# Optimization experiments

Hardware: AMD Instinct MI355X
Metric: run time of the kernel (lower is better)

The kernel has to match this reference:

```python
import jax, jax.numpy as jnp
import numpy as np

B, N, D, DHAT, H = 2, 2048, 1024, 512, 16
F = DHAT // H   # qk head dim = 32
G = D // H      # v head dim = 64


def setup_inputs() -> dict:
    key = jax.random.key(0)
    ks = jax.random.split(key, 9)
    def lin_w(k, din, dout):
        return jax.random.normal(k, (din, dout), jnp.float32) / np.sqrt(din).astype(np.float32)
    return {
        "x": jax.random.normal(ks[0], (B, N, D), jnp.float32),
        "wq": lin_w(ks[1], D, DHAT), "bq": jnp.zeros((DHAT,), jnp.float32),
        "wk": lin_w(ks[2], D, DHAT), "bk": jnp.zeros((DHAT,), jnp.float32),
        "wv": lin_w(ks[3], D, D),    "bv": jnp.zeros((D,), jnp.float32),
        "wo": lin_w(ks[4], D, D),    "bo": jnp.zeros((D,), jnp.float32),
    }


def _phi(x):
    # elu feature map: phi(x) = elu(x) + 1 (strictly positive)
    return jax.nn.elu(x) + 1.0


def _linear_attention(Q, K, V):
    # Q,K: (B,H,N,F); V: (B,H,N,G)
    kv = jnp.cumsum(jnp.einsum('bhtf,bhtg->bhtfg', K, V), axis=2)  # (B,H,N,F,G)
    Z = 1.0 / (jnp.einsum('bhtf,bhtf->bht', Q, jnp.cumsum(K, axis=2)) + 1e-6)
    out = jnp.einsum('bhtf,bhtfg->bhtg', Q, kv) * Z[..., None]     # (B,H,N,G)
    return out


def reference(x, wq, bq, wk, bk, wv, bv, wo, bo):
    Bx, Nx, Dx = x.shape
    Q = (x @ wq + bq).reshape(Bx, Nx, H, F).transpose(0, 2, 1, 3)  # (B,H,N,F)
    K = (x @ wk + bk).reshape(Bx, Nx, H, F).transpose(0, 2, 1, 3)
    V = (x @ wv + bv).reshape(Bx, Nx, H, G).transpose(0, 2, 1, 3)  # (B,H,N,G)
    Q, K = _phi(Q), _phi(K)
    out = _linear_attention(Q, K, V)                               # (B,H,N,G)
    out = out.transpose(0, 2, 1, 3).reshape(Bx, Nx, Dx)
    return out @ wo + bo
```

## Files before the change

### kernel.cpp

```cpp
#include <hip/hip_runtime.h>
#include <hip/hip_bf16.h>
#include <math.h>

#define B_    2
#define N_    2048
#define D_    1024
#define DHAT_ 512
#define H_    16
#define F_    32
#define G_    64
#define CHUNK 128
#define NCHUNK (N_ / CHUNK)
#define QKVLD 2048

typedef __attribute__((ext_vector_type(8))) short bf16x8;
typedef __attribute__((ext_vector_type(4))) float f32x4;

__device__ __forceinline__ float phi_fn(float x) {
    return x > 0.0f ? x + 1.0f : expf(x);
}

__device__ __forceinline__ ushort f2bf(float f) {
    unsigned u = __float_as_uint(f);
    u += 0x7FFFu + ((u >> 16) & 1u);
    return (ushort)(u >> 16);
}

__device__ __forceinline__ float bf2f(ushort u) {
    return __uint_as_float(((unsigned)u) << 16);
}

#define GLOAD_LDS16(g, l) __builtin_amdgcn_global_load_lds( \
    (const __attribute__((address_space(1))) void*)(g),     \
    (__attribute__((address_space(3))) void*)(l), 16, 0, 0)

__device__ __forceinline__ int sw64(int row) { return (row & 3) ^ ((row >> 2) & 3); }
__device__ __forceinline__ int swP(int t) { return (t & 7) ^ (((t >> 3) & 1) << 1); }

__device__ __forceinline__ void transpose_tile(
    const float* __restrict__ W, ushort* __restrict__ Wt,
    int K, int N, int bx, int by, int tid, ushort (*tile)[33])
{
    const int ti = by * 32, tj = bx * 32;
    const int tx = tid & 31, ty = tid >> 5;
    #pragma unroll
    for (int r = 0; r < 4; ++r)
        tile[ty + r * 8][tx] = f2bf(W[(size_t)(ti + ty + r * 8) * N + tj + tx]);
    __syncthreads();
    #pragma unroll
    for (int r = 0; r < 4; ++r)
        Wt[(size_t)(tj + ty + r * 8) * K + ti + tx] = tile[tx][ty + r * 8];
}

__global__ __launch_bounds__(256) void prep_kernel(
    const float* __restrict__ x,
    const float* __restrict__ wq, const float* __restrict__ wk,
    const float* __restrict__ wv, const float* __restrict__ wo,
    const float* __restrict__ bq, const float* __restrict__ bk,
    const float* __restrict__ bv,
    ushort* __restrict__ xbf, ushort* __restrict__ wqkvT,
    ushort* __restrict__ wot, float* __restrict__ bqkv)
{
    __shared__ ushort tile[32][33];
    const int id = blockIdx.x, tid = threadIdx.x;

    if (id < 4096) {
        int i = id * 256 + tid;
        float4 a = reinterpret_cast<const float4*>(x)[i];
        ushort4 o;
        o.x = f2bf(a.x); o.y = f2bf(a.y); o.z = f2bf(a.z); o.w = f2bf(a.w);
        reinterpret_cast<ushort4*>(xbf)[i] = o;
    } else if (id < 4608) {
        int tt = id - 4096;
        transpose_tile(wq, wqkvT, D_, DHAT_, tt & 15, tt >> 4, tid, tile);
    } else if (id < 5120) {
        int tt = id - 4608;
        transpose_tile(wk, wqkvT + (size_t)DHAT_ * D_, D_, DHAT_, tt & 15, tt >> 4, tid, tile);
    } else if (id < 6144) {
        int tt = id - 5120;
        transpose_tile(wv, wqkvT + (size_t)2 * DHAT_ * D_, D_, D_, tt & 31, tt >> 5, tid, tile);
    } else if (id < 7168) {
        int tt = id - 6144;
        transpose_tile(wo, wot, D_, D_, tt & 31, tt >> 5, tid, tile);
    } else {
        int i = (id - 7168) * 256 + tid;
        float v;
        if (i < DHAT_)          v = bq[i];
        else if (i < 2 * DHAT_) v = bk[i - DHAT_];
        else                    v = bv[i - 2 * DHAT_];
        bqkv[i] = v;
    }
}

template<bool OUTBF, int BN>
__global__ __launch_bounds__(256) void mfma_gemm_kernel(
    const ushort* __restrict__ A, const ushort* __restrict__ Wt,
    const float* __restrict__ bias, void* __restrict__ Cout,
    int M, int K, int N, int phi_upto)
{
    constexpr int NF = BN / 32;
    __shared__ __attribute__((aligned(16))) ushort Asm[128 * 32];
    __shared__ __attribute__((aligned(16))) ushort Bsm[BN * 32];

    const int tid  = threadIdx.x;
    const int lane = tid & 63;
    const int wave = tid >> 6;
    const int wr   = wave >> 1, wc = wave & 1;

    const int nwg  = gridDim.x * gridDim.y;
    const int flat = blockIdx.y * gridDim.x + blockIdx.x;
    const int cpx  = nwg >> 3;
    const int swz  = (flat & 7) * cpx + (flat >> 3);
    const int bx   = swz % gridDim.x, by = swz / gridDim.x;

    const int brow = by * 128, bcol = bx * BN;
    const int l16  = lane & 15, lk = lane >> 4;

    f32x4 acc[4][NF];
    #pragma unroll
    for (int m = 0; m < 4; ++m)
        #pragma unroll
        for (int n = 0; n < NF; ++n)
            acc[m][n] = (f32x4){0.f, 0.f, 0.f, 0.f};

    for (int k0 = 0; k0 < K; k0 += 32) {
        __syncthreads();
        #pragma unroll
        for (int r = 0; r < 2; ++r) {
            int fi  = r * 256 + tid;
            int row = fi >> 2;
            int c8  = (fi & 3) << 3;
            GLOAD_LDS16(&A[(size_t)(brow + row) * K + k0 + c8], &Asm[fi * 8]);
        }
        #pragma unroll
        for (int r = 0; r < BN / 64; ++r) {
            int fi  = r * 256 + tid;
            int row = fi >> 2;
            int c8  = (fi & 3) << 3;
            GLOAD_LDS16(&Wt[(size_t)(bcol + row) * K + k0 + c8], &Bsm[fi * 8]);
        }
        __syncthreads();

        bf16x8 af[4], bf[NF];
        #pragma unroll
        for (int m = 0; m < 4; ++m)
            af[m] = *reinterpret_cast<const bf16x8*>(&Asm[(wr * 64 + m * 16 + l16) * 32 + lk * 8]);
        #pragma unroll
        for (int n = 0; n < NF; ++n)
            bf[n] = *reinterpret_cast<const bf16x8*>(&Bsm[(wc * (BN / 2) + n * 16 + l16) * 32 + lk * 8]);
        #pragma unroll
        for (int m = 0; m < 4; ++m)
            #pragma unroll
            for (int n = 0; n < NF; ++n)
                acc[m][n] = __builtin_amdgcn_mfma_f32_16x16x32_bf16(af[m], bf[n], acc[m][n], 0, 0, 0);
    }

    #pragma unroll
    for (int n = 0; n < NF; ++n) {
        int col = bcol + wc * (BN / 2) + n * 16 + l16;
        float bv = bias[col];
        const bool do_phi = col < phi_upto;
        #pragma unroll
        for (int m = 0; m < 4; ++m) {
            int row0 = brow + wr * 64 + m * 16 + lk * 4;
            #pragma unroll
            for (int j = 0; j < 4; ++j) {
                float v = acc[m][n][j] + bv;
                if (do_phi) v = phi_fn(v);
                if (OUTBF)
                    ((ushort*)Cout)[(size_t)(row0 + j) * N + col] = f2bf(v);
                else
                    ((float*)Cout)[(size_t)(row0 + j) * N + col] = v;
            }
        }
    }
}

__global__ __launch_bounds__(256) void chunk_kv_kernel(
    const ushort* __restrict__ QKV, float* __restrict__ Sb, float* __restrict__ zb)
{
    __shared__ __attribute__((aligned(16))) ushort KsT[32 * 128];
    __shared__ __attribute__((aligned(16))) ushort VsT[64 * 128];

    const int c = blockIdx.x, h = blockIdx.y, b = blockIdx.z;
    const int tid = threadIdx.x;
    const int lane = tid & 63, wave = tid >> 6;
    const int l16 = lane & 15, lk = lane >> 4;
    const size_t row0 = (size_t)b * N_ + (size_t)c * CHUNK;

    #pragma unroll
    for (int r = 0; r < 2; ++r) {
        int fi = r * 256 + tid;
        int t = fi >> 2, f8 = (fi & 3) << 3;
        bf16x8 v = *reinterpret_cast<const bf16x8*>(&QKV[(row0 + t) * QKVLD + DHAT_ + h * F_ + f8]);
        #pragma unroll
        for (int i = 0; i < 8; ++i) {
            int f = f8 + i;
            KsT[f * 128 + (t ^ ((f & 7) << 3))] = (ushort)v[i];
        }
    }
    {
        int s = tid & 127, gh = tid >> 7;
        const ushort* vsrc = &QKV[(row0 + s) * QKVLD + 2 * DHAT_ + h * G_ + gh * 32];
        #pragma unroll
        for (int w = 0; w < 4; ++w) {
            bf16x8 v = *reinterpret_cast<const bf16x8*>(&vsrc[w * 8]);
            #pragma unroll
            for (int i = 0; i < 8; ++i) {
                int g = gh * 32 + w * 8 + i;
                VsT[g * 128 + (s ^ ((g & 7) << 3))] = (ushort)v[i];
            }
        }
    }
    __syncthreads();

    f32x4 sacc[2];
    sacc[0] = (f32x4){0.f, 0.f, 0.f, 0.f};
    sacc[1] = (f32x4){0.f, 0.f, 0.f, 0.f};
    const int g = wave * 16 + l16;
    #pragma unroll
    for (int ks = 0; ks < 4; ++ks) {
        int sl = ks * 4 + lk;
        bf16x8 bv = *reinterpret_cast<const bf16x8*>(&VsT[g * 128 + ((sl ^ (g & 7)) << 3)]);
        #pragma unroll
        for (int m = 0; m < 2; ++m) {
            int f = m * 16 + l16;
            bf16x8 ak = *reinterpret_cast<const bf16x8*>(&KsT[f * 128 + ((sl ^ (f & 7)) << 3)]);
            sacc[m] = __builtin_amdgcn_mfma_f32_16x16x32_bf16(ak, bv, sacc[m], 0, 0, 0);
        }
    }

    const size_t sbase = ((size_t)((b * H_ + h) * NCHUNK + c)) * (F_ * G_);
    #pragma unroll
    for (int m = 0; m < 2; ++m)
        #pragma unroll
        for (int j = 0; j < 4; ++j) {
            int f = m * 16 + lk * 4 + j;
            Sb[sbase + (size_t)f * G_ + g] = sacc[m][j];
        }

    {
        int f = tid >> 3, i = tid & 7;
        float zs = 0.0f;
        #pragma unroll
        for (int ss = 0; ss < 2; ++ss) {
            int sl = i * 2 + ss;
            bf16x8 kv = *reinterpret_cast<const bf16x8*>(&KsT[f * 128 + ((sl ^ (f & 7)) << 3)]);
            #pragma unroll
            for (int e = 0; e < 8; ++e) zs += bf2f((ushort)kv[e]);
        }
        zs += __shfl_xor(zs, 1);
        zs += __shfl_xor(zs, 2);
        zs += __shfl_xor(zs, 4);
        if (i == 0) zb[((size_t)(b * H_ + h) * NCHUNK + c) * F_ + f] = zs;
    }
}

__global__ __launch_bounds__(256) void scan_kernel(
    const float* __restrict__ Sb, ushort* __restrict__ SbT, float* __restrict__ zb)
{
    const int bh = blockIdx.x;
    const int tid = threadIdx.x;
    const int g = tid >> 2, f0 = (tid & 3) << 3;

    float p[8] = {};
    for (int c = 0; c < NCHUNK; ++c) {
        const size_t sbase = ((size_t)bh * NCHUNK + c) * (F_ * G_);
        float t[8];
        #pragma unroll
        for (int i = 0; i < 8; ++i) t[i] = Sb[sbase + (size_t)(f0 + i) * G_ + g];
        bf16x8 w;
        #pragma unroll
        for (int i = 0; i < 8; ++i) w[i] = (short)f2bf(p[i]);
        *reinterpret_cast<bf16x8*>(&SbT[(((size_t)bh * NCHUNK + c) * G_ + g) * F_ + f0]) = w;
        #pragma unroll
        for (int i = 0; i < 8; ++i) p[i] += t[i];
    }
    if (tid < F_) {
        float pz = 0.0f;
        for (int c = 0; c < NCHUNK; ++c) {
            size_t base = ((size_t)bh * NCHUNK + c) * F_ + tid;
            float t = zb[base];
            zb[base] = pz;
            pz += t;
        }
    }
}

__global__ __launch_bounds__(256) void attn_mfma_kernel(
    const ushort* __restrict__ QKV, const ushort* __restrict__ SbT,
    const float* __restrict__ zb, ushort* __restrict__ Obf)
{
    __shared__ __attribute__((aligned(16))) ushort Qs[128 * 32];
    __shared__ __attribute__((aligned(16))) ushort Ks[128 * 32];
    __shared__ __attribute__((aligned(16))) ushort VsT[64 * 128];
    __shared__ __attribute__((aligned(16))) ushort Ss[64 * 32];
    __shared__ __attribute__((aligned(16))) ushort Ps[128 * 128];
    __shared__ float zl[F_];
    __shared__ float denl[CHUNK];

    const int c = blockIdx.x, h = blockIdx.y, b = blockIdx.z;
    const int tid = threadIdx.x;
    const int lane = tid & 63, wave = tid >> 6;
    const int l16 = lane & 15, lk = lane >> 4;
    const size_t row0 = (size_t)b * N_ + (size_t)c * CHUNK;
    const int bh = b * H_ + h;

    #pragma unroll
    for (int r = 0; r < 2; ++r) {
        int fi = r * 256 + tid;
        int row = fi >> 2;
        int c8 = ((fi & 3) ^ sw64(row)) << 3;
        GLOAD_LDS16(&QKV[(row0 + row) * QKVLD + h * F_ + c8], &Qs[fi * 8]);
        GLOAD_LDS16(&QKV[(row0 + row) * QKVLD + DHAT_ + h * F_ + c8], &Ks[fi * 8]);
    }
    {
        int g = tid >> 2;
        int f8 = ((tid & 3) ^ sw64(g)) << 3;
        GLOAD_LDS16(&SbT[(((size_t)bh * NCHUNK + c) * G_ + g) * F_ + f8], &Ss[tid * 8]);
    }
    if (tid < F_) zl[tid] = zb[((size_t)bh * NCHUNK + c) * F_ + tid];
    {
        int s = tid & 127, gh = tid >> 7;
        const ushort* vsrc = &QKV[(row0 + s) * QKVLD + 2 * DHAT_ + h * G_ + gh * 32];
        #pragma unroll
        for (int w = 0; w < 4; ++w) {
            bf16x8 v = *reinterpret_cast<const bf16x8*>(&vsrc[w * 8]);
            #pragma unroll
            for (int i = 0; i < 8; ++i) {
                int g = gh * 32 + w * 8 + i;
                VsT[g * 128 + (s ^ ((g & 7) << 3))] = (ushort)v[i];
            }
        }
    }
    __syncthreads();

    const int mbase = wave * 32;

    bf16x8 aq[2];
    #pragma unroll
    for (int m = 0; m < 2; ++m) {
        int row = mbase + m * 16 + l16;
        aq[m] = *reinterpret_cast<const bf16x8*>(&Qs[row * 32 + ((lk ^ sw64(row)) << 3)]);
    }

    f32x4 p[2][8];
    #pragma unroll
    for (int m = 0; m < 2; ++m)
        #pragma unroll
        for (int n = 0; n < 8; ++n)
            p[m][n] = (f32x4){0.f, 0.f, 0.f, 0.f};
    #pragma unroll
    for (int n = 0; n < 8; ++n) {
        int srow = n * 16 + l16;
        bf16x8 bk = *reinterpret_cast<const bf16x8*>(&Ks[srow * 32 + ((lk ^ sw64(srow)) << 3)]);
        p[0][n] = __builtin_amdgcn_mfma_f32_16x16x32_bf16(aq[0], bk, p[0][n], 0, 0, 0);
        p[1][n] = __builtin_amdgcn_mfma_f32_16x16x32_bf16(aq[1], bk, p[1][n], 0, 0, 0);
    }

    #pragma unroll
    for (int m = 0; m < 2; ++m)
        #pragma unroll
        for (int n = 0; n < 8; ++n) {
            int s = n * 16 + l16;
            #pragma unroll
            for (int j = 0; j < 4; ++j) {
                int t = mbase + m * 16 + lk * 4 + j;
                float v = (s <= t) ? p[m][n][j] : 0.0f;
                Ps[t * 128 + ((s & 7) | (((s >> 3) ^ swP(t)) << 3))] = f2bf(v);
            }
        }

    {
        int t = tid >> 1, h2 = tid & 1;
        float rs = 0.0f;
        #pragma unroll
        for (int r = 0; r < 8; ++r) {
            int sl = h2 * 8 + r;
            bf16x8 pv = *reinterpret_cast<const bf16x8*>(&Ps[t * 128 + ((sl ^ swP(t)) << 3)]);
            #pragma unroll
            for (int i = 0; i < 8; ++i) rs += bf2f((ushort)pv[i]);
        }
        #pragma unroll
        for (int ss = 0; ss < 2; ++ss) {
            int sl = h2 * 2 + ss;
            bf16x8 qv = *reinterpret_cast<const bf16x8*>(&Qs[t * 32 + ((sl ^ sw64(t)) << 3)]);
            #pragma unroll
            for (int i = 0; i < 8; ++i) rs += bf2f((ushort)qv[i]) * zl[sl * 8 + i];
        }
        rs += __shfl_xor(rs, 1);
        if (h2 == 0) denl[t] = rs + 1e-6f;
    }

    f32x4 o[2][4];
    #pragma unroll
    for (int m = 0; m < 2; ++m)
        #pragma unroll
        for (int n = 0; n < 4; ++n)
            o[m][n] = (f32x4){0.f, 0.f, 0.f, 0.f};
    #pragma unroll
    for (int n = 0; n < 4; ++n) {
        int g = n * 16 + l16;
        bf16x8 bs = *reinterpret_cast<const bf16x8*>(&Ss[g * 32 + ((lk ^ sw64(g)) << 3)]);
        o[0][n] = __builtin_amdgcn_mfma_f32_16x16x32_bf16(aq[0], bs, o[0][n], 0, 0, 0);
        o[1][n] = __builtin_amdgcn_mfma_f32_16x16x32_bf16(aq[1], bs, o[1][n], 0, 0, 0);
    }
    #pragma unroll
    for (int ks = 0; ks < 4; ++ks) {
        bf16x8 ap[2];
        #pragma unroll
        for (int m = 0; m < 2; ++m) {
            int t = mbase + m * 16 + l16;
            int sl = ks * 4 + lk;
            ap[m] = *reinterpret_cast<const bf16x8*>(&Ps[t * 128 + ((sl ^ swP(t)) << 3)]);
        }
        #pragma unroll
        for (int n = 0; n < 4; ++n) {
            int g = n * 16 + l16;
            bf16x8 bv = *reinterpret_cast<const bf16x8*>(&VsT[g * 128 + (((ks * 4 + lk) ^ (g & 7)) << 3)]);
            o[0][n] = __builtin_amdgcn_mfma_f32_16x16x32_bf16(ap[0], bv, o[0][n], 0, 0, 0);
            o[1][n] = __builtin_amdgcn_mfma_f32_16x16x32_bf16(ap[1], bv, o[1][n], 0, 0, 0);
        }
    }

    #pragma unroll
    for (int m = 0; m < 2; ++m)
        #pragma unroll
        for (int j = 0; j < 4; ++j) {
            int t = mbase + m * 16 + lk * 4 + j;
            float rinv = 1.0f / denl[t];
            #pragma unroll
            for (int n = 0; n < 4; ++n) {
                int g = n * 16 + l16;
                Obf[(row0 + t) * D_ + h * G_ + g] = f2bf(o[m][n][j] * rinv);
            }
        }
}

extern "C" void kernel_launch(void* const* d_in, const int* in_sizes, int n_in,
                              void* d_out, int out_size, void* d_ws, size_t ws_size,
                              hipStream_t stream) {
    const float* x  = (const float*)d_in[0];
    const float* wq = (const float*)d_in[1];
    const float* bq = (const float*)d_in[2];
    const float* wk = (const float*)d_in[3];
    const float* bk = (const float*)d_in[4];
    const float* wv = (const float*)d_in[5];
    const float* bv = (const float*)d_in[6];
    const float* wo = (const float*)d_in[7];
    const float* bo = (const float*)d_in[8];
    float* out = (float*)d_out;

    size_t off = 0;
    char* base = (char*)d_ws;
    auto alloc = [&](size_t bytes) -> void* {
        void* p = base + off;
        off += (bytes + 255) & ~(size_t)255;
        return p;
    };
    const size_t MN = (size_t)B_ * N_;
    ushort* QKV   = (ushort*)alloc(MN * QKVLD * 2);
    float*  Sb    = (float*) alloc((size_t)B_ * H_ * NCHUNK * F_ * G_ * 4);
    ushort* SbT   = (ushort*)alloc((size_t)B_ * H_ * NCHUNK * G_ * F_ * 2);
    float*  zb    = (float*) alloc((size_t)B_ * H_ * NCHUNK * F_ * 4);
    ushort* xbf   = (ushort*)alloc(MN * D_ * 2);
    ushort* wqkvT = (ushort*)alloc((size_t)QKVLD * D_ * 2);
    ushort* wot   = (ushort*)alloc((size_t)D_ * D_ * 2);
    float*  bqkv  = (float*) alloc((size_t)QKVLD * 4);
    ushort* obf   = (ushort*)alloc(MN * D_ * 2);

    const int M = (int)MN;

    prep_kernel<<<dim3(7176), 256, 0, stream>>>(
        x, wq, wk, wv, wo, bq, bk, bv, xbf, wqkvT, wot, bqkv);

    mfma_gemm_kernel<true, 128><<<dim3(QKVLD / 128, M / 128), 256, 0, stream>>>(
        xbf, wqkvT, bqkv, QKV, M, D_, QKVLD, 2 * DHAT_);

    chunk_kv_kernel<<<dim3(NCHUNK, H_, B_), 256, 0, stream>>>(QKV, Sb, zb);
    scan_kernel<<<dim3(B_ * H_), 256, 0, stream>>>(Sb, SbT, zb);
    attn_mfma_kernel<<<dim3(NCHUNK, H_, B_), 256, 0, stream>>>(QKV, SbT, zb, obf);

    mfma_gemm_kernel<false, 64><<<dim3(D_ / 64, M / 128), 256, 0, stream>>>(
        obf, wot, bo, out, M, D_, D_, 0);
}
```

Measured before the change: 165.4 us.

## Fuse chunk prefix scan into attention kernel and widen GEMM K-tile with swizzle

Removes the separate scan kernel: each attention block now sums the fp32 per-chunk KV states and normalizer sums of all preceding chunks itself, then writes the bf16 prefix into shared memory. This drops one kernel launch and the SbT round trip. The cost is redundant reads that grow with the chunk index. Separately, the GEMM K-step is doubled to 64 with an XOR-swizzled shared-memory layout, which halves barrier count and is meant to cut LDS bank conflicts, at the cost of more shared memory per block.

```diff
diff --git a/kernel.cpp b/kernel.cpp
--- a/kernel.cpp
+++ b/kernel.cpp
@@ -99,8 +99,8 @@
     int M, int K, int N, int phi_upto)
 {
     constexpr int NF = BN / 32;
-    __shared__ __attribute__((aligned(16))) ushort Asm[128 * 32];
-    __shared__ __attribute__((aligned(16))) ushort Bsm[BN * 32];
+    __shared__ __attribute__((aligned(16))) ushort Asm[128 * 64];
+    __shared__ __attribute__((aligned(16))) ushort Bsm[BN * 64];
 
     const int tid  = threadIdx.x;
     const int lane = tid & 63;
@@ -123,36 +123,45 @@
         for (int n = 0; n < NF; ++n)
             acc[m][n] = (f32x4){0.f, 0.f, 0.f, 0.f};
 
-    for (int k0 = 0; k0 < K; k0 += 32) {
+    for (int k0 = 0; k0 < K; k0 += 64) {
         __syncthreads();
         #pragma unroll
-        for (int r = 0; r < 2; ++r) {
+        for (int r = 0; r < 4; ++r) {
             int fi  = r * 256 + tid;
-            int row = fi >> 2;
-            int c8  = (fi & 3) << 3;
-            GLOAD_LDS16(&A[(size_t)(brow + row) * K + k0 + c8], &Asm[fi * 8]);
-        }
-        #pragma unroll
-        for (int r = 0; r < BN / 64; ++r) {
+            int row = fi >> 3, sl = fi & 7;
+            GLOAD_LDS16(&A[(size_t)(brow + row) * K + k0 + ((sl ^ (row & 7)) << 3)],
+                        &Asm[fi * 8]);
+        }
+        #pragma unroll
+        for (int r = 0; r < BN / 32; ++r) {
             int fi  = r * 256 + tid;
-            int row = fi >> 2;
-            int c8  = (fi & 3) << 3;
-            GLOAD_LDS16(&Wt[(size_t)(bcol + row) * K + k0 + c8], &Bsm[fi * 8]);
+            int row = fi >> 3, sl = fi & 7;
+            GLOAD_LDS16(&Wt[(size_t)(bcol + row) * K + k0 + ((sl ^ (row & 7)) << 3)],
+                        &Bsm[fi * 8]);
         }
         __syncthreads();
 
-        bf16x8 af[4], bf[NF];
-        #pragma unroll
-        for (int m = 0; m < 4; ++m)
-            af[m] = *reinterpret_cast<const bf16x8*>(&Asm[(wr * 64 + m * 16 + l16) * 32 + lk * 8]);
-        #pragma unroll
-        for (int n = 0; n < NF; ++n)
-            bf[n] = *reinterpret_cast<const bf16x8*>(&Bsm[(wc * (BN / 2) + n * 16 + l16) * 32 + lk * 8]);
-        #pragma unroll
-        for (int m = 0; m < 4; ++m)
-            #pragma unroll
-            for (int n = 0; n < NF; ++n)
-                acc[m][n] = __builtin_amdgcn_mfma_f32_16x16x32_bf16(af[m], bf[n], acc[m][n], 0, 0, 0);
+        #pragma unroll
+        for (int kk = 0; kk < 2; ++kk) {
+            bf16x8 af[4], bf[NF];
+            #pragma unroll
+            for (int m = 0; m < 4; ++m) {
+                int row = wr * 64 + m * 16 + l16;
+                af[m] = *reinterpret_cast<const bf16x8*>(
+                    &Asm[row * 64 + (((kk * 4 + lk) ^ (row & 7)) << 3)]);
+            }
+            #pragma unroll
+            for (int n = 0; n < NF; ++n) {
+                int row = wc * (BN / 2) + n * 16 + l16;
+                bf[n] = *reinterpret_cast<const bf16x8*>(
+                    &Bsm[row * 64 + (((kk * 4 + lk) ^ (row & 7)) << 3)]);
+            }
+            #pragma unroll
+            for (int m = 0; m < 4; ++m)
+                #pragma unroll
+                for (int n = 0; n < NF; ++n)
+                    acc[m][n] = __builtin_amdgcn_mfma_f32_16x16x32_bf16(af[m], bf[n], acc[m][n], 0, 0, 0);
+        }
     }
 
     #pragma unroll
@@ -256,39 +265,8 @@
     }
 }
 
-__global__ __launch_bounds__(256) void scan_kernel(
-    const float* __restrict__ Sb, ushort* __restrict__ SbT, float* __restrict__ zb)
-{
-    const int bh = blockIdx.x;
-    const int tid = threadIdx.x;
-    const int g = tid >> 2, f0 = (tid & 3) << 3;
-
-    float p[8] = {};
-    for (int c = 0; c < NCHUNK; ++c) {
-        const size_t sbase = ((size_t)bh * NCHUNK + c) * (F_ * G_);
-        float t[8];
-        #pragma unroll
-        for (int i = 0; i < 8; ++i) t[i] = Sb[sbase + (size_t)(f0 + i) * G_ + g];
-        bf16x8 w;
-        #pragma unroll
-        for (int i = 0; i < 8; ++i) w[i] = (short)f2bf(p[i]);
-        *reinterpret_cast<bf16x8*>(&SbT[(((size_t)bh * NCHUNK + c) * G_ + g) * F_ + f0]) = w;
-        #pragma unroll
-        for (int i = 0; i < 8; ++i) p[i] += t[i];
-    }
-    if (tid < F_) {
-        float pz = 0.0f;
-        for (int c = 0; c < NCHUNK; ++c) {
-            size_t base = ((size_t)bh * NCHUNK + c) * F_ + tid;
-            float t = zb[base];
-            zb[base] = pz;
-            pz += t;
-        }
-    }
-}
-
 __global__ __launch_bounds__(256) void attn_mfma_kernel(
-    const ushort* __restrict__ QKV, const ushort* __restrict__ SbT,
+    const ushort* __restrict__ QKV, const float* __restrict__ Sb,
     const float* __restrict__ zb, ushort* __restrict__ Obf)
 {
     __shared__ __attribute__((aligned(16))) ushort Qs[128 * 32];
@@ -315,11 +293,24 @@
         GLOAD_LDS16(&QKV[(row0 + row) * QKVLD + DHAT_ + h * F_ + c8], &Ks[fi * 8]);
     }
     {
-        int g = tid >> 2;
-        int f8 = ((tid & 3) ^ sw64(g)) << 3;
-        GLOAD_LDS16(&SbT[(((size_t)bh * NCHUNK + c) * G_ + g) * F_ + f8], &Ss[tid * 8]);
-    }
-    if (tid < F_) zl[tid] = zb[((size_t)bh * NCHUNK + c) * F_ + tid];
+        int g = tid >> 2, f0 = (tid & 3) << 3;
+        float s[8] = {};
+        for (int cc = 0; cc < c; ++cc) {
+            const float* sp = &Sb[((size_t)bh * NCHUNK + cc) * (F_ * G_)];
+            #pragma unroll
+            for (int i = 0; i < 8; ++i) s[i] += sp[(size_t)(f0 + i) * G_ + g];
+        }
+        bf16x8 w;
+        #pragma unroll
+        for (int i = 0; i < 8; ++i) w[i] = (short)f2bf(s[i]);
+        *reinterpret_cast<bf16x8*>(&Ss[g * 32 + ((((f0 >> 3)) ^ sw64(g)) << 3)]) = w;
+    }
+    if (tid < F_) {
+        float pz = 0.0f;
+        for (int cc = 0; cc < c; ++cc)
+            pz += zb[((size_t)bh * NCHUNK + cc) * F_ + tid];
+        zl[tid] = pz;
+    }
     {
         int s = tid & 127, gh = tid >> 7;
         const ushort* vsrc = &QKV[(row0 + s) * QKVLD + 2 * DHAT_ + h * G_ + gh * 32];
@@ -461,7 +452,6 @@
     const size_t MN = (size_t)B_ * N_;
     ushort* QKV   = (ushort*)alloc(MN * QKVLD * 2);
     float*  Sb    = (float*) alloc((size_t)B_ * H_ * NCHUNK * F_ * G_ * 4);
-    ushort* SbT   = (ushort*)alloc((size_t)B_ * H_ * NCHUNK * G_ * F_ * 2);
     float*  zb    = (float*) alloc((size_t)B_ * H_ * NCHUNK * F_ * 4);
     ushort* xbf   = (ushort*)alloc(MN * D_ * 2);
     ushort* wqkvT = (ushort*)alloc((size_t)QKVLD * D_ * 2);
@@ -478,8 +468,7 @@
         xbf, wqkvT, bqkv, QKV, M, D_, QKVLD, 2 * DHAT_);
 
     chunk_kv_kernel<<<dim3(NCHUNK, H_, B_), 256, 0, stream>>>(QKV, Sb, zb);
-    scan_kernel<<<dim3(B_ * H_), 256, 0, stream>>>(Sb, SbT, zb);
-    attn_mfma_kernel<<<dim3(NCHUNK, H_, B_), 256, 0, stream>>>(QKV, SbT, zb, obf);
+    attn_mfma_kernel<<<dim3(NCHUNK, H_, B_), 256, 0, stream>>>(QKV, Sb, zb, obf);
 
     mfma_gemm_kernel<false, 64><<<dim3(D_ / 64, M / 128), 256, 0, stream>>>(
         obf, wot, bo, out, M, D_, D_, 0);
```

Result: faster. 156.4 us (-5.5%).
